# Kernel tuning notes

Measured on AMD Instinct MI355X. Metric: run time of the kernel, lower is better.

## Reference

```python
import jax, jax.numpy as jnp
import numpy as np

N_SRC, N_DST, K, T = 16384, 8192, 16, 2
NODE_IN, EDGE_IN, TIME_D = 128, 64, 128
D_MODEL = NODE_IN + TIME_D + EDGE_IN  # 320
N_HEAD, D_K = 8, 64                   # d_k = d_v
HID = 128
LN_EPS = 1e-5


def setup_inputs() -> dict:
    key = jax.random.key(0)
    ks = jax.random.split(key, 10)
    std_qk = np.sqrt(2.0 / (D_MODEL + D_K)).astype(np.float32)
    return {
        "node_features": jax.random.normal(ks[0], (N_SRC, NODE_IN), jnp.float32),
        "edge_features": jax.random.normal(ks[1], (N_DST, K, T, EDGE_IN), jnp.float32),
        "delta_t": jax.random.uniform(ks[2], (N_DST, K, T), jnp.float32) * 100.0,
        "neigh_idx": jax.random.randint(ks[3], (N_DST, K), 0, N_SRC),
        "basis_freq": jnp.asarray(1.0 / 10 ** np.linspace(0, 9, TIME_D), jnp.float32),
        "phase": jnp.zeros((TIME_D,), jnp.float32),
        "w_qs": jax.random.normal(ks[4], (N_HEAD * D_K, D_MODEL), jnp.float32) * std_qk,
        "w_ks": jax.random.normal(ks[5], (N_HEAD * D_K, D_MODEL), jnp.float32) * std_qk,
        "w_vs": jax.random.normal(ks[6], (N_HEAD * D_K, D_MODEL), jnp.float32) * std_qk,
        "fc_w": jax.random.normal(ks[7], (D_MODEL, N_HEAD * D_K), jnp.float32) * 0.03,
        "fc_b": jnp.zeros((D_MODEL,), jnp.float32),
        "ln_g": jnp.ones((D_MODEL,), jnp.float32),
        "ln_b": jnp.zeros((D_MODEL,), jnp.float32),
        "node_w": jax.random.normal(ks[8], (HID, 2 * NODE_IN + TIME_D + EDGE_IN), jnp.float32) * 0.05,
        "node_b": jnp.zeros((HID,), jnp.float32),
    }


def reference(node_features, edge_features, delta_t, neigh_idx, basis_freq, phase,
              w_qs, w_ks, w_vs, fc_w, fc_b, ln_g, ln_b, node_w, node_b):
    h_dst = node_features[:N_DST]                                  # [N, NODE_IN]
    # message_func: per-edge time encoding + gather src feats + concat
    te = jnp.cos(delta_t[..., None] * basis_freq + phase)          # [N, K, T, TIME_D]
    h_nb = node_features[neigh_idx]                                # [N, K, NODE_IN] (irregular gather)
    h_nb = jnp.broadcast_to(h_nb[:, :, None, :], (N_DST, K, T, NODE_IN))
    m = jnp.concatenate([h_nb, edge_features, te], axis=-1)        # [N, K, T, D_MODEL]
    m = m.reshape(N_DST, K * T, D_MODEL)                           # mailbox kv
    # reduce_func query: [h_dst, zeros(edge_in), time_encode(0)=cos(phase)]
    t0 = jnp.broadcast_to(jnp.cos(phase), (N_DST, TIME_D))
    q = jnp.concatenate([h_dst, jnp.zeros((N_DST, EDGE_IN), h_dst.dtype), t0], axis=-1)  # [N, D_MODEL]
    # multi-head attention (len_q = 1)
    qh = (q @ w_qs.T).reshape(N_DST, N_HEAD, D_K)
    kh = (m @ w_ks.T).reshape(N_DST, K * T, N_HEAD, D_K)
    vh = (m @ w_vs.T).reshape(N_DST, K * T, N_HEAD, D_K)
    scores = jnp.einsum('nhd,nlhd->nhl', qh, kh) / np.float32(np.sqrt(D_K))
    attn = jax.nn.softmax(scores, axis=-1)
    ctx = jnp.einsum('nhl,nlhd->nhd', attn, vh).reshape(N_DST, N_HEAD * D_K)
    out = ctx @ fc_w.T + fc_b
    x = out + q                                                    # residual
    mu = x.mean(-1, keepdims=True)
    var = x.var(-1, keepdims=True)
    h_neigh = ln_g * (x - mu) * jax.lax.rsqrt(var + LN_EPS) + ln_b  # layer norm
    h = jnp.concatenate([h_dst, h_neigh], axis=-1)                 # [N, 2*NODE_IN+TIME_D+EDGE_IN]
    return jax.nn.relu(h @ node_w.T + node_b)                      # [N, HID]
```

## Files before the change

kernel.cpp:

```cpp
#include <hip/hip_runtime.h>
#include <math.h>

#define LNB      32
#define NODE_IN  128
#define EDGE_IN  64
#define TIME_D   128
#define D_MODEL  320
#define N_HEAD   8
#define D_K      64
#define NHD      512
#define HID      128
#define IN2      448
#define N_DSTN   8192

typedef __attribute__((ext_vector_type(8))) short bf16x8;
typedef __attribute__((ext_vector_type(4))) float f32x4;
#define MFMA16(a,b,c) __builtin_amdgcn_mfma_f32_16x16x32_bf16(a,b,c,0,0,0)

#define WS_QKM   0
#define WS_WQK   20971520
#define WS_WVF   21299200
#define WS_NWC   22118400
#define WS_F32   22175744
#define WS_X     22182784

#define F_C0     0
#define F_C0K    512
#define F_CC     3072
#define F_B2     3392

__device__ __forceinline__ unsigned short f2bf(float f) {
  __bf16 h = (__bf16)f;
  return __builtin_bit_cast(unsigned short, h);
}
__device__ __forceinline__ bf16x8 pack8(const float* v) {
  unsigned short b8[8];
  #pragma unroll
  for (int j = 0; j < 8; ++j) b8[j] = f2bf(v[j]);
  return *(const bf16x8*)b8;
}

__global__ __launch_bounds__(256)
void prep1a(const float* __restrict__ nw, const float* __restrict__ lng,
            const float* __restrict__ fcb, const float* __restrict__ ph,
            unsigned short* __restrict__ ws)
{
  int i = blockIdx.x * 256 + threadIdx.x;
  unsigned short* nwc = ws + WS_NWC;
  float* f32r = (float*)(ws + WS_F32);
  if (i < 16384) {
    int o = i >> 7, k = i & 127;
    nwc[o * IN2 + k] = f2bf(nw[(size_t)o * IN2 + k]);
  } else if (i < 57344) {
    int j = i - 16384, o = j / 320, c = j - o * 320;
    nwc[o * IN2 + 128 + c] = f2bf(nw[(size_t)o * IN2 + 128 + c] * lng[c]);
  } else if (i < 57664) {
    int c = i - 57344;
    f32r[F_CC + c] = fcb[c] + (c >= 192 ? __cosf(ph[c - 192]) : 0.f);
  }
}

__global__ __launch_bounds__(256)
void prep1b(const float* __restrict__ wq, const float* __restrict__ ph,
            const float* __restrict__ nw, const float* __restrict__ lnb_,
            const float* __restrict__ nb, unsigned short* __restrict__ ws)
{
  float* f32r = (float*)(ws + WS_F32);
  int gw = (blockIdx.x * 256 + threadIdx.x) >> 6;
  int ln = threadIdx.x & 63;
  if (gw < 512) {
    float s = __cosf(ph[ln])      * wq[(size_t)gw * D_MODEL + 192 + ln]
            + __cosf(ph[ln + 64]) * wq[(size_t)gw * D_MODEL + 256 + ln];
    #pragma unroll
    for (int off = 32; off >= 1; off >>= 1) s += __shfl_xor(s, off);
    if (ln == 0) f32r[F_C0 + gw] = s;
  } else {
    int o = gw - 512;
    float s = 0.f;
    #pragma unroll
    for (int k = 0; k < 5; ++k) {
      int c = ln + 64 * k;
      s += nw[(size_t)o * IN2 + 128 + c] * lnb_[c];
    }
    #pragma unroll
    for (int off = 32; off >= 1; off >>= 1) s += __shfl_xor(s, off);
    if (ln == 0) f32r[F_B2 + o] = nb[o] + s;
  }
}

__global__ __launch_bounds__(256)
void prep_c0k(const float* __restrict__ wk, unsigned short* __restrict__ ws)
{
  float* f32r = (float*)(ws + WS_F32);
  int gw = (blockIdx.x * 256 + threadIdx.x) >> 6;
  int ln = threadIdx.x & 63;
  int h = gw / 320, d = gw - h * 320;
  float s = f32r[F_C0 + h * 64 + ln] * wk[(size_t)(h * 64 + ln) * D_MODEL + d];
  #pragma unroll
  for (int off = 32; off >= 1; off >>= 1) s += __shfl_xor(s, off);
  if (ln == 0) f32r[F_C0K + gw] = s;
}

__global__ __launch_bounds__(256)
void prep_wqk(const float* __restrict__ wq, const float* __restrict__ wk,
              unsigned short* __restrict__ ws)
{
  __shared__ float sQw[64 * 128];
  __shared__ float sKw[64 * 32];
  int h = blockIdx.x / 10, d0 = (blockIdx.x - h * 10) * 32;
  int tid = threadIdx.x;
  #pragma unroll 4
  for (int it = 0; it < 32; ++it) {
    int idx = it * 256 + tid;
    int r = idx >> 7, c = idx & 127;
    sQw[idx] = wq[(size_t)(h * 64 + r) * D_MODEL + c];
  }
  #pragma unroll
  for (int it = 0; it < 8; ++it) {
    int idx = it * 256 + tid;
    int r = idx >> 5, c = idx & 31;
    sKw[idx] = wk[(size_t)(h * 64 + r) * D_MODEL + d0 + c];
  }
  __syncthreads();
  int di = tid >> 3, k0 = (tid & 7) * 16;
  float acc[16] = {};
  for (int dk = 0; dk < 64; ++dk) {
    float w = sKw[dk * 32 + di];
    #pragma unroll
    for (int j = 0; j < 16; ++j) acc[j] += w * sQw[dk * 128 + k0 + j];
  }
  unsigned short* dst = ws + WS_WQK + (size_t)(h * 320 + d0 + di) * 128 + k0;
  #pragma unroll
  for (int j = 0; j < 16; ++j) dst[j] = f2bf(acc[j]);
}

__global__ __launch_bounds__(256)
void prep_wvf(const float* __restrict__ fcw, const float* __restrict__ wv,
              unsigned short* __restrict__ ws)
{
  __shared__ float sF[32 * 64];
  __shared__ float sW[64 * 32];
  int b = blockIdx.x;
  int h = b / 100, r2 = b - h * 100;
  int ct = r2 / 10;
  int c0 = ct * 32, d0 = (r2 - ct * 10) * 32;
  int tid = threadIdx.x;
  #pragma unroll
  for (int it = 0; it < 8; ++it) {
    int idx = it * 256 + tid;
    int i = idx >> 6, jj = idx & 63;
    sF[idx] = fcw[(size_t)(c0 + i) * NHD + h * 64 + jj];
  }
  #pragma unroll
  for (int it = 0; it < 8; ++it) {
    int idx = it * 256 + tid;
    int jj = idx >> 5, i = idx & 31;
    sW[idx] = wv[(size_t)(h * 64 + jj) * D_MODEL + d0 + i];
  }
  __syncthreads();
  int ci = tid >> 3, dj0 = (tid & 7) * 4;
  float acc[4] = {};
  for (int jj = 0; jj < 64; ++jj) {
    float f = sF[ci * 64 + jj];
    #pragma unroll
    for (int k = 0; k < 4; ++k) acc[k] += f * sW[jj * 32 + dj0 + k];
  }
  unsigned short* wvf = ws + WS_WVF;
  #pragma unroll
  for (int k = 0; k < 4; ++k)
    wvf[(size_t)(c0 + ci) * 2560 + (size_t)(d0 + dj0 + k) * 8 + h] = f2bf(acc[k]);
}

__global__ __launch_bounds__(256, 6)
void tgat_qk(const float* __restrict__ nf, const unsigned short* __restrict__ ws,
             unsigned short* __restrict__ qkm)
{
  __shared__ alignas(16) unsigned short sA[64 * 136];
  const int tid = threadIdx.x, wid = tid >> 6, lane = tid & 63, qd = lane >> 4, lm = lane & 15;
  const int mt_blk = blockIdx.x / 20, nt_blk = blockIdx.x - mt_blk * 20;
  const int n0 = mt_blk * 64, c0 = nt_blk * 128;
  const unsigned short* wqk = ws + WS_WQK;
  const float* f32r = (const float*)(ws + WS_F32);

  {
    int n = tid >> 2, k0 = (tid & 3) * 32;
    const float4* src = (const float4*)(nf + (size_t)(n0 + n) * NODE_IN + k0);
    #pragma unroll
    for (int q = 0; q < 4; ++q) {
      float4 f0 = src[2 * q], f1 = src[2 * q + 1];
      float v[8] = {f0.x, f0.y, f0.z, f0.w, f1.x, f1.y, f1.z, f1.w};
      *(bf16x8*)&sA[n * 136 + k0 + q * 8] = pack8(v);
    }
  }
  __syncthreads();

  f32x4 acc[2][4] = {};
  for (int kt = 0; kt < 4; ++kt) {
    bf16x8 a[4];
    #pragma unroll
    for (int mt = 0; mt < 4; ++mt)
      a[mt] = *(const bf16x8*)&sA[(mt * 16 + lm) * 136 + kt * 32 + qd * 8];
    #pragma unroll
    for (int t = 0; t < 2; ++t) {
      int cg = c0 + (2 * wid + t) * 16 + lm;
      bf16x8 b = *(const bf16x8*)&wqk[(size_t)cg * 128 + kt * 32 + qd * 8];
      #pragma unroll
      for (int mt = 0; mt < 4; ++mt) acc[t][mt] = MFMA16(a[mt], b, acc[t][mt]);
    }
  }
  #pragma unroll
  for (int t = 0; t < 2; ++t) {
    int cg = c0 + (2 * wid + t) * 16 + lm;
    float ck = f32r[F_C0K + cg];
    #pragma unroll
    for (int mt = 0; mt < 4; ++mt)
      #pragma unroll
      for (int r = 0; r < 4; ++r)
        qkm[(size_t)(n0 + mt * 16 + qd * 4 + r) * 2560 + cg] = f2bf(acc[t][mt][r] + ck);
  }
}

__global__ __launch_bounds__(256, 6)
void tgat_attn(const float* __restrict__ nf, const float* __restrict__ ef,
               const float* __restrict__ dtp, const int* __restrict__ nidx,
               const float* __restrict__ freq, const float* __restrict__ ph,
               unsigned short* __restrict__ qkm)
{
  __shared__ alignas(16) unsigned short sM[LNB * 328];
  __shared__ alignas(16) unsigned short sATT[16 * 40];

  const int tid = threadIdx.x;
  const int wid = tid >> 6, lane = tid & 63, qd = lane >> 4, lm = lane & 15;
  const int n = blockIdx.x;
  unsigned short* qn = qkm + (size_t)n * 2560;

  #pragma unroll 1
  for (int it = 0; it < 5; ++it) {
    int g = it * 256 + tid;
    int l = g & 31, dg = g >> 5;
    int d0 = dg * 8;
    float v[8];
    if (dg < 16) {
      int ni = nidx[n * 16 + (l >> 1)];
      const float4* src = (const float4*)(nf + (size_t)ni * NODE_IN + d0);
      float4 f0 = src[0], f1 = src[1];
      v[0]=f0.x; v[1]=f0.y; v[2]=f0.z; v[3]=f0.w; v[4]=f1.x; v[5]=f1.y; v[6]=f1.z; v[7]=f1.w;
    } else if (dg < 24) {
      const float4* src = (const float4*)(ef + ((size_t)n * LNB + l) * EDGE_IN + (d0 - NODE_IN));
      float4 f0 = src[0], f1 = src[1];
      v[0]=f0.x; v[1]=f0.y; v[2]=f0.z; v[3]=f0.w; v[4]=f1.x; v[5]=f1.y; v[6]=f1.z; v[7]=f1.w;
    } else {
      int dd = d0 - 192;
      float dt = dtp[(size_t)n * LNB + l];
      const float4* fq = (const float4*)(freq + dd);
      const float4* pp = (const float4*)(ph + dd);
      float4 q0 = fq[0], q1 = fq[1], p0 = pp[0], p1 = pp[1];
      v[0] = __cosf(dt * q0.x + p0.x); v[1] = __cosf(dt * q0.y + p0.y);
      v[2] = __cosf(dt * q0.z + p0.z); v[3] = __cosf(dt * q0.w + p0.w);
      v[4] = __cosf(dt * q1.x + p1.x); v[5] = __cosf(dt * q1.y + p1.y);
      v[6] = __cosf(dt * q1.z + p1.z); v[7] = __cosf(dt * q1.w + p1.w);
    }
    *(bf16x8*)&sM[l * 328 + d0] = pack8(v);
  }

  bf16x8 qfrag[10];
  if (wid == 0) {
    #pragma unroll
    for (int kt = 0; kt < 10; ++kt) {
      qfrag[kt] = (bf16x8){0,0,0,0,0,0,0,0};
      if (lm < 8) qfrag[kt] = *(const bf16x8*)&qn[lm * 320 + kt * 32 + qd * 8];
    }
  }
  __syncthreads();

  const int tbeg = (wid == 0) ? 0 : 2 + (wid - 1) * 6;
  const int tcnt = (wid == 0) ? 2 : 6;
  bf16x8 afr[6];

  if (wid == 0) {
    f32x4 acc0 = {}, acc1 = {};
    #pragma unroll
    for (int kt = 0; kt < 10; ++kt) {
      bf16x8 a0 = *(const bf16x8*)&sM[lm * 328 + kt * 32 + qd * 8];
      bf16x8 a1 = *(const bf16x8*)&sM[(16 + lm) * 328 + kt * 32 + qd * 8];
      acc0 = MFMA16(a0, qfrag[kt], acc0);
      acc1 = MFMA16(a1, qfrag[kt], acc1);
    }
    float s[8], e[8];
    #pragma unroll
    for (int r = 0; r < 4; ++r) { s[r] = acc0[r] * 0.125f; s[4 + r] = acc1[r] * 0.125f; }
    float mx = s[0];
    #pragma unroll
    for (int i = 1; i < 8; ++i) mx = fmaxf(mx, s[i]);
    mx = fmaxf(mx, __shfl_xor(mx, 16));
    mx = fmaxf(mx, __shfl_xor(mx, 32));
    float sum = 0.f;
    #pragma unroll
    for (int i = 0; i < 8; ++i) { e[i] = __expf(s[i] - mx); sum += e[i]; }
    sum += __shfl_xor(sum, 16);
    sum += __shfl_xor(sum, 32);
    float inv = 1.f / sum;
    #pragma unroll
    for (int i = 0; i < 8; ++i) {
      int l = (i < 4) ? (qd * 4 + i) : (16 + qd * 4 + (i - 4));
      sATT[lm * 40 + l] = f2bf(e[i] * inv);
    }
  } else {
    #pragma unroll
    for (int u = 0; u < 6; ++u) {
      int d = (tbeg + u) * 16 + lm;
      unsigned short a8[8];
      #pragma unroll
      for (int j = 0; j < 8; ++j) a8[j] = sM[(qd * 8 + j) * 328 + d];
      afr[u] = *(const bf16x8*)a8;
    }
  }
  __syncthreads();

  if (wid == 0) {
    #pragma unroll
    for (int u = 0; u < 2; ++u) {
      int d = u * 16 + lm;
      unsigned short a8[8];
      #pragma unroll
      for (int j = 0; j < 8; ++j) a8[j] = sM[(qd * 8 + j) * 328 + d];
      afr[u] = *(const bf16x8*)a8;
    }
  }
  bf16x8 batt = *(const bf16x8*)&sATT[lm * 40 + qd * 8];
  #pragma unroll
  for (int u = 0; u < 6; ++u) {
    if (u < tcnt) {
      int dtile = tbeg + u;
      f32x4 acc = {};
      acc = MFMA16(afr[u], batt, acc);
      if (lm < 8) {
        #pragma unroll
        for (int r = 0; r < 4; ++r)
          qn[(dtile * 16 + qd * 4 + r) * 8 + lm] = f2bf(acc[r]);
      }
    }
  }
}

__global__ __launch_bounds__(256)
void tgat_xgemm(const unsigned short* __restrict__ ws,
                const unsigned short* __restrict__ qkm, float* __restrict__ xacc)
{
  __shared__ alignas(16) unsigned short sA[64 * 136];
  const int tid = threadIdx.x, wid = tid >> 6, lane = tid & 63, qd = lane >> 4, lm = lane & 15;
  const int s = blockIdx.x >> 7, mb = blockIdx.x & 127;
  const int n0 = mb * 64, k0 = s * 640;
  const unsigned short* wvf = ws + WS_WVF;

  f32x4 acc[4][5] = {};
  for (int kc = 0; kc < 5; ++kc) {
    __syncthreads();
    {
      int n = tid >> 2, p = (tid & 3) * 32;
      const unsigned short* src = qkm + (size_t)(n0 + n) * 2560 + k0 + kc * 128 + p;
      *(bf16x8*)&sA[n * 136 + p]      = *(const bf16x8*)(src);
      *(bf16x8*)&sA[n * 136 + p + 8]  = *(const bf16x8*)(src + 8);
      *(bf16x8*)&sA[n * 136 + p + 16] = *(const bf16x8*)(src + 16);
      *(bf16x8*)&sA[n * 136 + p + 24] = *(const bf16x8*)(src + 24);
    }
    __syncthreads();
    #pragma unroll
    for (int kt = 0; kt < 4; ++kt) {
      bf16x8 b[5];
      #pragma unroll
      for (int u = 0; u < 5; ++u) {
        int c = wid * 80 + u * 16 + lm;
        b[u] = *(const bf16x8*)&wvf[(size_t)c * 2560 + k0 + kc * 128 + kt * 32 + qd * 8];
      }
      #pragma unroll
      for (int mt = 0; mt < 4; ++mt) {
        bf16x8 a = *(const bf16x8*)&sA[(mt * 16 + lm) * 136 + kt * 32 + qd * 8];
        #pragma unroll
        for (int u = 0; u < 5; ++u) acc[mt][u] = MFMA16(a, b[u], acc[mt][u]);
      }
    }
  }
  #pragma unroll
  for (int mt = 0; mt < 4; ++mt)
    #pragma unroll
    for (int u = 0; u < 5; ++u) {
      int c = wid * 80 + u * 16 + lm;
      #pragma unroll
      for (int r = 0; r < 4; ++r)
        atomicAdd(&xacc[(size_t)(n0 + mt * 16 + qd * 4 + r) * 320 + c], acc[mt][u][r]);
    }
}

__global__ __launch_bounds__(256, 4)
void tgat_post2(const float* __restrict__ nf, const unsigned short* __restrict__ ws,
                const float* __restrict__ xacc, float* __restrict__ out)
{
  __shared__ alignas(16) unsigned short sQb[16 * 136];
  __shared__ alignas(16) unsigned short sXb[16 * 328];
  const int tid = threadIdx.x, wid = tid >> 6, lane = tid & 63, qd = lane >> 4, lm = lane & 15;
  const int n0 = blockIdx.x * 16;
  const unsigned short* nwc = ws + WS_NWC;
  const float* f32r = (const float*)(ws + WS_F32);

  {
    int nn = tid >> 4, kk = (tid & 15) * 8;
    const float4* src = (const float4*)(nf + (size_t)(n0 + nn) * NODE_IN + kk);
    float4 f0 = src[0], f1 = src[1];
    float v8[8] = {f0.x, f0.y, f0.z, f0.w, f1.x, f1.y, f1.z, f1.w};
    *(bf16x8*)&sQb[nn * 136 + kk] = pack8(v8);
  }
  const int rr = tid >> 4, cl = tid & 15;
  float v[20], s1 = 0.f, s2 = 0.f;
  #pragma unroll
  for (int u = 0; u < 20; ++u) {
    int c = u * 16 + cl;
    float x = xacc[(size_t)(n0 + rr) * 320 + c] + f32r[F_CC + c];
    if (c < 128) x += nf[(size_t)(n0 + rr) * NODE_IN + c];
    v[u] = x; s1 += x; s2 += x * x;
  }
  #pragma unroll
  for (int off = 8; off >= 1; off >>= 1) { s1 += __shfl_xor(s1, off); s2 += __shfl_xor(s2, off); }
  float mean = s1 * (1.f / D_MODEL);
  float var  = s2 * (1.f / D_MODEL) - mean * mean;
  float rstd = rsqrtf(var + 1e-5f);
  #pragma unroll
  for (int u = 0; u < 20; ++u) {
    int c = u * 16 + cl;
    sXb[rr * 328 + c] = f2bf((v[u] - mean) * rstd);
  }
  __syncthreads();

  #pragma unroll
  for (int t = 0; t < 2; ++t) {
    int o = (wid * 2 + t) * 16 + lm;
    f32x4 acc = {};
    for (int kt = 0; kt < 14; ++kt) {
      bf16x8 a;
      if (kt < 4) a = *(const bf16x8*)&sQb[lm * 136 + kt * 32 + qd * 8];
      else        a = *(const bf16x8*)&sXb[lm * 328 + (kt - 4) * 32 + qd * 8];
      bf16x8 b = *(const bf16x8*)&nwc[(size_t)o * IN2 + kt * 32 + qd * 8];
      acc = MFMA16(a, b, acc);
    }
    float bz = f32r[F_B2 + o];
    #pragma unroll
    for (int r = 0; r < 4; ++r)
      out[(size_t)(n0 + qd * 4 + r) * HID + o] = fmaxf(acc[r] + bz, 0.f);
  }
}

extern "C" void kernel_launch(void* const* d_in, const int* in_sizes, int n_in,
                              void* d_out, int out_size, void* d_ws, size_t ws_size,
                              hipStream_t stream) {
  const float* nf   = (const float*)d_in[0];
  const float* ef   = (const float*)d_in[1];
  const float* dtp  = (const float*)d_in[2];
  const int*   nidx = (const int*)  d_in[3];
  const float* freq = (const float*)d_in[4];
  const float* ph   = (const float*)d_in[5];
  const float* wq   = (const float*)d_in[6];
  const float* wk   = (const float*)d_in[7];
  const float* wv   = (const float*)d_in[8];
  const float* fcw  = (const float*)d_in[9];
  const float* fcb  = (const float*)d_in[10];
  const float* lng  = (const float*)d_in[11];
  const float* lnb_ = (const float*)d_in[12];
  const float* nw   = (const float*)d_in[13];
  const float* nb   = (const float*)d_in[14];
  float* out = (float*)d_out;
  unsigned short* ws = (unsigned short*)d_ws;
  unsigned short* qkm = ws + WS_QKM;
  float* xacc = (float*)(ws + WS_X);

  hipMemsetAsync(xacc, 0, (size_t)N_DSTN * D_MODEL * sizeof(float), stream);
  prep1a  <<<226, 256, 0, stream>>>(nw, lng, fcb, ph, ws);
  prep1b  <<<160, 256, 0, stream>>>(wq, ph, nw, lnb_, nb, ws);
  prep_c0k<<<640, 256, 0, stream>>>(wk, ws);
  prep_wqk<<<80,  256, 0, stream>>>(wq, wk, ws);
  prep_wvf<<<800, 256, 0, stream>>>(fcw, wv, ws);
  tgat_qk   <<<2560, 256, 0, stream>>>(nf, ws, qkm);
  tgat_attn <<<8192, 256, 0, stream>>>(nf, ef, dtp, nidx, freq, ph, qkm);
  tgat_xgemm<<<512,  256, 0, stream>>>(ws, qkm, xacc);
  tgat_post2<<<512,  256, 0, stream>>>(nf, ws, xacc, out);
}
```

Measured before the change: 283.5 us.

## Restructure xgemm to split N across blocks and reduce K in-block, dropping atomics

The xgemm kernel previously split the K dimension across four blocks per row tile and merged partial sums with float atomicAdd into a memset-zeroed buffer. Now each 512-thread block owns an 80-column slice and covers the whole K range. Its two wave groups each handle half of K and are combined through shared memory before a plain store. This removes the memset and the atomic traffic, at the cost of more shared memory per block, fewer MFMAs per A-fragment load, and the 64-row A tile being reloaded for each of the four column slices.

```diff
diff --git a/kernel.cpp b/kernel.cpp
--- a/kernel.cpp
+++ b/kernel.cpp
@@ -343,53 +343,64 @@
   }
 }
 
-__global__ __launch_bounds__(256)
+__global__ __launch_bounds__(512, 4)
 void tgat_xgemm(const unsigned short* __restrict__ ws,
                 const unsigned short* __restrict__ qkm, float* __restrict__ xacc)
 {
-  __shared__ alignas(16) unsigned short sA[64 * 136];
-  const int tid = threadIdx.x, wid = tid >> 6, lane = tid & 63, qd = lane >> 4, lm = lane & 15;
-  const int s = blockIdx.x >> 7, mb = blockIdx.x & 127;
-  const int n0 = mb * 64, k0 = s * 640;
+  __shared__ alignas(16) unsigned short sA[2][64 * 136];
+  __shared__ float sRed[64 * 80];
+  const int tid = threadIdx.x, wid = tid >> 6, lane = tid & 63;
+  const int qd = lane >> 4, lm = lane & 15;
+  const int ns = blockIdx.x >> 7, mb = blockIdx.x & 127;
+  const int n0 = mb * 64, c0 = ns * 80;
+  const int kh = wid >> 2, wm = wid & 3;
   const unsigned short* wvf = ws + WS_WVF;
 
-  f32x4 acc[4][5] = {};
-  for (int kc = 0; kc < 5; ++kc) {
+  const int sb = tid >> 8, tt = tid & 255;
+  const int srow = tt >> 2, sp = (tt & 3) * 32;
+
+  f32x4 acc[5] = {};
+  for (int it = 0; it < 10; ++it) {
     __syncthreads();
     {
-      int n = tid >> 2, p = (tid & 3) * 32;
-      const unsigned short* src = qkm + (size_t)(n0 + n) * 2560 + k0 + kc * 128 + p;
-      *(bf16x8*)&sA[n * 136 + p]      = *(const bf16x8*)(src);
-      *(bf16x8*)&sA[n * 136 + p + 8]  = *(const bf16x8*)(src + 8);
-      *(bf16x8*)&sA[n * 136 + p + 16] = *(const bf16x8*)(src + 16);
-      *(bf16x8*)&sA[n * 136 + p + 24] = *(const bf16x8*)(src + 24);
+      const unsigned short* src =
+          qkm + (size_t)(n0 + srow) * 2560 + sb * 1280 + it * 128 + sp;
+      *(bf16x8*)&sA[sb][srow * 136 + sp]      = *(const bf16x8*)(src);
+      *(bf16x8*)&sA[sb][srow * 136 + sp + 8]  = *(const bf16x8*)(src + 8);
+      *(bf16x8*)&sA[sb][srow * 136 + sp + 16] = *(const bf16x8*)(src + 16);
+      *(bf16x8*)&sA[sb][srow * 136 + sp + 24] = *(const bf16x8*)(src + 24);
     }
     __syncthreads();
     #pragma unroll
     for (int kt = 0; kt < 4; ++kt) {
-      bf16x8 b[5];
+      bf16x8 a = *(const bf16x8*)&sA[kh][(wm * 16 + lm) * 136 + kt * 32 + qd * 8];
       #pragma unroll
       for (int u = 0; u < 5; ++u) {
-        int c = wid * 80 + u * 16 + lm;
-        b[u] = *(const bf16x8*)&wvf[(size_t)c * 2560 + k0 + kc * 128 + kt * 32 + qd * 8];
+        int c = c0 + u * 16 + lm;
+        bf16x8 b = *(const bf16x8*)
+            &wvf[(size_t)c * 2560 + kh * 1280 + it * 128 + kt * 32 + qd * 8];
+        acc[u] = MFMA16(a, b, acc[u]);
       }
-      #pragma unroll
-      for (int mt = 0; mt < 4; ++mt) {
-        bf16x8 a = *(const bf16x8*)&sA[(mt * 16 + lm) * 136 + kt * 32 + qd * 8];
-        #pragma unroll
-        for (int u = 0; u < 5; ++u) acc[mt][u] = MFMA16(a, b[u], acc[mt][u]);
+    }
+  }
+  __syncthreads();
+  if (kh == 1) {
+    #pragma unroll
+    for (int u = 0; u < 5; ++u)
+      #pragma unroll
+      for (int r = 0; r < 4; ++r)
+        sRed[(wm * 16 + qd * 4 + r) * 80 + u * 16 + lm] = acc[u][r];
+  }
+  __syncthreads();
+  if (kh == 0) {
+    #pragma unroll
+    for (int u = 0; u < 5; ++u)
+      #pragma unroll
+      for (int r = 0; r < 4; ++r) {
+        float v = acc[u][r] + sRed[(wm * 16 + qd * 4 + r) * 80 + u * 16 + lm];
+        xacc[(size_t)(n0 + wm * 16 + qd * 4 + r) * 320 + c0 + u * 16 + lm] = v;
       }
-    }
-  }
-  #pragma unroll
-  for (int mt = 0; mt < 4; ++mt)
-    #pragma unroll
-    for (int u = 0; u < 5; ++u) {
-      int c = wid * 80 + u * 16 + lm;
-      #pragma unroll
-      for (int r = 0; r < 4; ++r)
-        atomicAdd(&xacc[(size_t)(n0 + mt * 16 + qd * 4 + r) * 320 + c], acc[mt][u][r]);
-    }
+  }
 }
 
 __global__ __launch_bounds__(256, 4)
@@ -472,7 +483,6 @@
   unsigned short* qkm = ws + WS_QKM;
   float* xacc = (float*)(ws + WS_X);
 
-  hipMemsetAsync(xacc, 0, (size_t)N_DSTN * D_MODEL * sizeof(float), stream);
   prep1a  <<<226, 256, 0, stream>>>(nw, lng, fcb, ph, ws);
   prep1b  <<<160, 256, 0, stream>>>(wq, ph, nw, lnb_, nb, ws);
   prep_c0k<<<640, 256, 0, stream>>>(wk, ws);
@@ -480,6 +490,6 @@
   prep_wvf<<<800, 256, 0, stream>>>(fcw, wv, ws);
   tgat_qk   <<<2560, 256, 0, stream>>>(nf, ws, qkm);
   tgat_attn <<<8192, 256, 0, stream>>>(nf, ef, dtp, nidx, freq, ph, qkm);
-  tgat_xgemm<<<512,  256, 0, stream>>>(ws, qkm, xacc);
+  tgat_xgemm<<<512,  512, 0, stream>>>(ws, qkm, xacc);
   tgat_post2<<<512,  256, 0, stream>>>(nf, ws, xacc, out);
 }
```

New measurement: 325.2 us. 1.15x slower.
